# Performance work log

Hardware: AMD Instinct MI355X
Metric: run time of the kernel (lower is better)

The kernel has to match this reference:

```python
import jax, jax.numpy as jnp
import numpy as np

N_INIT = jnp.array([17.047, 14.099, 3.625], dtype=jnp.float32)
CA_INIT = jnp.array([16.967, 12.784, 4.338], dtype=jnp.float32)
C_INIT = jnp.array([15.685, 12.755, 5.133], dtype=jnp.float32)


def _unit(x):
    return x / (jnp.linalg.norm(x, axis=-1, keepdims=True) + 1e-8)


def _place_dihedral(a, b, c, bond_angle, bond_length, torsion):
    # a,b,c: [B,3]; bond_angle/bond_length/torsion: [B]
    ab = b - a
    bc = _unit(c - b)
    cr = jnp.cross(ab, bc)
    crn = jnp.linalg.norm(cr, axis=-1, keepdims=True)
    n_main = _unit(cr)
    # collinear fallback (per-element; almost never triggers for real angles)
    perp = jnp.zeros_like(bc).at[..., 0].set(1.0)
    ct = jnp.cross(bc, perp)
    ctn = jnp.linalg.norm(ct, axis=-1, keepdims=True)
    perp2 = jnp.where(ctn < 1e-6, jnp.zeros_like(bc).at[..., 1].set(1.0), perp)
    n_fb = _unit(jnp.cross(bc, perp2))
    n = jnp.where(crn < 1e-6, n_fb, n_main)
    nbc = jnp.cross(n, bc)
    m = jnp.stack([bc, nbc, n], axis=-1)  # [B,3,3]
    d_local = jnp.stack([
        -bond_length * jnp.cos(bond_angle),
        bond_length * jnp.cos(torsion) * jnp.sin(bond_angle),
        bond_length * jnp.sin(torsion) * jnp.sin(bond_angle),
    ], axis=-1)  # [B,3]
    d = jnp.einsum('bij,bj->bi', m, d_local)
    return d + c


def _nerf_build(phi, psi, omega, bond_lengths, bond_angles):
    B, L = phi.shape
    init = jnp.broadcast_to(jnp.stack([N_INIT, CA_INIT, C_INIT]), (B, 3, 3))
    # per-step params, leading axis = residue index i in [0, L-2]
    xs = (
        psi[:, :L - 1].T,                 # psi_i
        omega[:, :L - 1].T,               # omega_i
        phi[:, 1:].T,                     # phi_{i+1}
        bond_lengths[:, :L - 1, 2].T,     # C-N length
        bond_lengths[:, :L - 1, 0].T,     # N-CA length
        bond_lengths[:, :L - 1, 1].T,     # CA-C length
        bond_angles[:, :L - 1, 1].T,      # CA-C-N angle
        bond_angles[:, :L - 1, 2].T,      # C-N-CA angle
        bond_angles[:, :L - 1, 0].T,      # N-CA-C angle
    )

    def step(prev, x):
        psi_i, omega_i, phi_i, len_cn, len_nca, len_cac, ang_cacn, ang_cnca, ang_ncac = x
        a, b, c = prev[:, 0], prev[:, 1], prev[:, 2]
        n = _place_dihedral(a, b, c, ang_cacn, len_cn, psi_i)
        ca = _place_dihedral(b, c, n, ang_cnca, len_nca, omega_i)
        cc = _place_dihedral(c, n, ca, ang_ncac, len_cac, phi_i)
        new = jnp.stack([n, ca, cc], axis=1)  # [B,3,3]
        return new, new

    _, outs = jax.lax.scan(step, init, xs)  # [L-1,B,3,3]
    rest = outs.transpose(1, 0, 2, 3).reshape(B, 3 * (L - 1), 3)
    return jnp.concatenate([init, rest], axis=1)  # [B, 3L, 3]


def setup_inputs() -> dict:
    key = jax.random.key(0)
    k0, k1, k2, k3, k4 = jax.random.split(key, 5)
    B, L = 4096, 512
    phi = jax.random.normal(k0, (B, L), dtype=jnp.float32)
    psi = jax.random.normal(k1, (B, L), dtype=jnp.float32)
    omega = jax.random.normal(k2, (B, L), dtype=jnp.float32)
    # realistic positive bond lengths (~1.0-1.5 A) and bond angles (~1.5-2.3 rad)
    bond_lengths = 1.0 + 0.5 * jax.random.uniform(k3, (B, L, 3), dtype=jnp.float32)
    bond_angles = 1.5 + 0.8 * jax.random.uniform(k4, (B, L, 3), dtype=jnp.float32)
    return {"phi": phi, "psi": psi, "omega": omega,
            "bond_lengths": bond_lengths, "bond_angles": bond_angles}


def reference(phi, psi, omega, bond_lengths, bond_angles):
    return _nerf_build(phi, psi, omega, bond_lengths, bond_angles)
```

## Files before the change

kernel.cpp:

```cpp
#include <hip/hip_runtime.h>
#include <math.h>


struct Xform { float r[9]; float t[3]; };

__device__ __forceinline__ void xf_identity(Xform& A) {
  A.r[0]=1.f; A.r[1]=0.f; A.r[2]=0.f;
  A.r[3]=0.f; A.r[4]=1.f; A.r[5]=0.f;
  A.r[6]=0.f; A.r[7]=0.f; A.r[8]=1.f;
  A.t[0]=0.f; A.t[1]=0.f; A.t[2]=0.f;
}

__device__ __forceinline__ Xform xf_compose(const Xform& A, const Xform& B) {
  Xform C;
#pragma unroll
  for (int i = 0; i < 3; ++i) {
    float a0 = A.r[3*i+0], a1 = A.r[3*i+1], a2 = A.r[3*i+2];
    C.r[3*i+0] = a0*B.r[0] + a1*B.r[3] + a2*B.r[6];
    C.r[3*i+1] = a0*B.r[1] + a1*B.r[4] + a2*B.r[7];
    C.r[3*i+2] = a0*B.r[2] + a1*B.r[5] + a2*B.r[8];
    C.t[i]     = a0*B.t[0] + a1*B.t[1] + a2*B.t[2] + A.t[i];
  }
  return C;
}

__device__ __forceinline__ Xform xf_delta(float theta, float len, float tau) {
  float st, ct, sx, cx;
  __sincosf(theta, &st, &ct);
  __sincosf(tau, &sx, &cx);
  float ux = -ct, uy = cx*st, uz = sx*st;
  Xform D;
  D.r[0] = ux;     D.r[1] = -st;    D.r[2] = 0.f;
  D.r[3] = uy;     D.r[4] = -ct*cx; D.r[5] = -sx;
  D.r[6] = uz;     D.r[7] = -ct*sx; D.r[8] = cx;
  D.t[0] = len*ux; D.t[1] = len*uy; D.t[2] = len*uz;
  return D;
}

__device__ __forceinline__ void xf_store(float* p, const Xform& A) {
#pragma unroll
  for (int i = 0; i < 9; ++i) p[i] = A.r[i];
#pragma unroll
  for (int i = 0; i < 3; ++i) p[9+i] = A.t[i];
}
__device__ __forceinline__ void xf_load(const float* p, Xform& A) {
#pragma unroll
  for (int i = 0; i < 9; ++i) A.r[i] = p[i];
#pragma unroll
  for (int i = 0; i < 3; ++i) A.t[i] = p[9+i];
}

#define LCH 512
#define NRES 511
#define SCAN_STRIDE 13

static __device__ const float c_init[9] = {
  17.047f, 14.099f, 3.625f,
  16.967f, 12.784f, 4.338f,
  15.685f, 12.755f, 5.133f };

__global__ __launch_bounds__(256) void nerf_scan_kernel(
    const float* __restrict__ g_phi, const float* __restrict__ g_psi,
    const float* __restrict__ g_omg, const float* __restrict__ g_bl,
    const float* __restrict__ g_ba, float* __restrict__ g_out)
{
  __shared__ float s_psi[NRES];
  __shared__ float s_omg[NRES];
  __shared__ float s_phi[NRES];
  __shared__ float s_bl[3*NRES];
  __shared__ float s_ba[3*NRES];
  __shared__ float s_scan[256*SCAN_STRIDE];

  const int b = blockIdx.x;
  const int t = threadIdx.x;

  const float* phir = g_phi + (size_t)b*LCH;
  const float* psir = g_psi + (size_t)b*LCH;
  const float* omgr = g_omg + (size_t)b*LCH;
  const float* blr  = g_bl  + (size_t)b*LCH*3;
  const float* bar  = g_ba  + (size_t)b*LCH*3;

  for (int i = t; i < NRES; i += 256) {
    s_psi[i] = psir[i];
    s_omg[i] = omgr[i];
    s_phi[i] = phir[i+1];
  }
  for (int i = t; i < 3*NRES; i += 256) {
    s_bl[i] = blr[i];
    s_ba[i] = bar[i];
  }
  __syncthreads();

  Xform P; xf_identity(P);
#pragma unroll
  for (int e = 0; e < 2; ++e) {
    int j = 2*t + e;
    if (j < NRES) {
      P = xf_compose(P, xf_delta(s_ba[3*j+1], s_bl[3*j+2], s_psi[j]));
      P = xf_compose(P, xf_delta(s_ba[3*j+2], s_bl[3*j+0], s_omg[j]));
      P = xf_compose(P, xf_delta(s_ba[3*j+0], s_bl[3*j+1], s_phi[j]));
    }
  }
  xf_store(&s_scan[t*SCAN_STRIDE], P);
  __syncthreads();

  for (int d = 1; d < 256; d <<= 1) {
    Xform left;
    bool act = (t >= d);
    if (act) xf_load(&s_scan[(t-d)*SCAN_STRIDE], left);
    __syncthreads();
    if (act) {
      P = xf_compose(left, P);
      xf_store(&s_scan[t*SCAN_STRIDE], P);
    }
    __syncthreads();
  }

  Xform A;
  {
    const float ax=17.047f, ay=14.099f, az=3.625f;
    const float bx_=16.967f, by_=12.784f, bz_=4.338f;
    const float cx_=15.685f, cy_=12.755f, cz_=5.133f;
    float abx=bx_-ax, aby=by_-ay, abz=bz_-az;
    float vx=cx_-bx_, vy=cy_-by_, vz=cz_-bz_;
    float vn = sqrtf(vx*vx+vy*vy+vz*vz) + 1e-8f;
    vx/=vn; vy/=vn; vz/=vn;
    float crx = aby*vz - abz*vy;
    float cry = abz*vx - abx*vz;
    float crz = abx*vy - aby*vx;
    float cn = sqrtf(crx*crx+cry*cry+crz*crz) + 1e-8f;
    float nx=crx/cn, ny=cry/cn, nz=crz/cn;
    float mx = ny*vz - nz*vy;
    float my = nz*vx - nx*vz;
    float mz = nx*vy - ny*vx;
    Xform I0;
    I0.r[0]=vx; I0.r[1]=mx; I0.r[2]=nx;
    I0.r[3]=vy; I0.r[4]=my; I0.r[5]=ny;
    I0.r[6]=vz; I0.r[7]=mz; I0.r[8]=nz;
    I0.t[0]=cx_; I0.t[1]=cy_; I0.t[2]=cz_;
    if (t == 0) {
      A = I0;
    } else {
      Xform E; xf_load(&s_scan[(t-1)*SCAN_STRIDE], E);
      A = xf_compose(I0, E);
    }
  }

  float* orow = g_out + (size_t)b * (3*LCH) * 3;
  if (t < 9) orow[t] = c_init[t];

#pragma unroll
  for (int e = 0; e < 2; ++e) {
    int j = 2*t + e;
    if (j < NRES) {
      float* o = orow + (size_t)(3 + 3*j) * 3;
      A = xf_compose(A, xf_delta(s_ba[3*j+1], s_bl[3*j+2], s_psi[j]));
      o[0]=A.t[0]; o[1]=A.t[1]; o[2]=A.t[2];
      A = xf_compose(A, xf_delta(s_ba[3*j+2], s_bl[3*j+0], s_omg[j]));
      o[3]=A.t[0]; o[4]=A.t[1]; o[5]=A.t[2];
      A = xf_compose(A, xf_delta(s_ba[3*j+0], s_bl[3*j+1], s_phi[j]));
      o[6]=A.t[0]; o[7]=A.t[1]; o[8]=A.t[2];
    }
  }
}

extern "C" void kernel_launch(void* const* d_in, const int* in_sizes, int n_in,
                              void* d_out, int out_size, void* d_ws, size_t ws_size,
                              hipStream_t stream) {
  const float* phi = (const float*)d_in[0];
  const float* psi = (const float*)d_in[1];
  const float* omg = (const float*)d_in[2];
  const float* bl  = (const float*)d_in[3];
  const float* ba  = (const float*)d_in[4];
  float* out = (float*)d_out;
  const int B = in_sizes[0] / LCH;
  hipLaunchKernelGGL(nerf_scan_kernel, dim3(B), dim3(256), 0, stream,
                     phi, psi, omg, bl, ba, out);
}
```

Baseline: 168.6 us.

## Map one chain per wavefront with register-resident inputs and shuffle-based scan

Each 64-lane wavefront now handles a whole chain, with 8 residues per lane, instead of one 256-thread block per chain. Inputs are loaded with float4 into registers, and the block-level LDS scan with barriers is replaced by a wave-level scan using __shfl_up. Composing with each elementary transform is specialised into an in-place step that exploits the known zero entry. Each lane now does a serial chain of 24 steps twice, which raises register pressure and serial latency. Output stores per lane are strided rather than coalesced.

```diff
diff --git a/kernel.cpp b/kernel.cpp
--- a/kernel.cpp
+++ b/kernel.cpp
@@ -2,17 +2,14 @@
 #include <math.h>
 
 
-struct Xform { float r[9]; float t[3]; };
+#define LCH 512
+#define NRES 511
+#define RPL 8
 
-__device__ __forceinline__ void xf_identity(Xform& A) {
-  A.r[0]=1.f; A.r[1]=0.f; A.r[2]=0.f;
-  A.r[3]=0.f; A.r[4]=1.f; A.r[5]=0.f;
-  A.r[6]=0.f; A.r[7]=0.f; A.r[8]=1.f;
-  A.t[0]=0.f; A.t[1]=0.f; A.t[2]=0.f;
-}
+struct Xf { float r[9]; float t[3]; };
 
-__device__ __forceinline__ Xform xf_compose(const Xform& A, const Xform& B) {
-  Xform C;
+__device__ __forceinline__ Xf xf_compose(const Xf& A, const Xf& B) {
+  Xf C;
 #pragma unroll
   for (int i = 0; i < 3; ++i) {
     float a0 = A.r[3*i+0], a1 = A.r[3*i+1], a2 = A.r[3*i+2];
@@ -24,99 +21,121 @@
   return C;
 }
 
-__device__ __forceinline__ Xform xf_delta(float theta, float len, float tau) {
+__device__ __forceinline__ void xf_step(Xf& P, float theta, float len, float tau) {
   float st, ct, sx, cx;
   __sincosf(theta, &st, &ct);
   __sincosf(tau, &sx, &cx);
   float ux = -ct, uy = cx*st, uz = sx*st;
-  Xform D;
-  D.r[0] = ux;     D.r[1] = -st;    D.r[2] = 0.f;
-  D.r[3] = uy;     D.r[4] = -ct*cx; D.r[5] = -sx;
-  D.r[6] = uz;     D.r[7] = -ct*sx; D.r[8] = cx;
-  D.t[0] = len*ux; D.t[1] = len*uy; D.t[2] = len*uz;
-  return D;
+  float v0 = -st, v1 = -ct*cx, v2 = -ct*sx;
+  float c00 = P.r[0]*ux + P.r[1]*uy + P.r[2]*uz;
+  float c10 = P.r[3]*ux + P.r[4]*uy + P.r[5]*uz;
+  float c20 = P.r[6]*ux + P.r[7]*uy + P.r[8]*uz;
+  float c01 = P.r[0]*v0 + P.r[1]*v1 + P.r[2]*v2;
+  float c11 = P.r[3]*v0 + P.r[4]*v1 + P.r[5]*v2;
+  float c21 = P.r[6]*v0 + P.r[7]*v1 + P.r[8]*v2;
+  float c02 = P.r[2]*cx - P.r[1]*sx;
+  float c12 = P.r[5]*cx - P.r[4]*sx;
+  float c22 = P.r[8]*cx - P.r[7]*sx;
+  P.t[0] += len*c00; P.t[1] += len*c10; P.t[2] += len*c20;
+  P.r[0]=c00; P.r[1]=c01; P.r[2]=c02;
+  P.r[3]=c10; P.r[4]=c11; P.r[5]=c12;
+  P.r[6]=c20; P.r[7]=c21; P.r[8]=c22;
 }
 
-__device__ __forceinline__ void xf_store(float* p, const Xform& A) {
-#pragma unroll
-  for (int i = 0; i < 9; ++i) p[i] = A.r[i];
-#pragma unroll
-  for (int i = 0; i < 3; ++i) p[9+i] = A.t[i];
-}
-__device__ __forceinline__ void xf_load(const float* p, Xform& A) {
-#pragma unroll
-  for (int i = 0; i < 9; ++i) A.r[i] = p[i];
-#pragma unroll
-  for (int i = 0; i < 3; ++i) A.t[i] = p[9+i];
+__device__ __forceinline__ void xf_set_delta(Xf& P, float theta, float len, float tau) {
+  float st, ct, sx, cx;
+  __sincosf(theta, &st, &ct);
+  __sincosf(tau, &sx, &cx);
+  float ux = -ct, uy = cx*st, uz = sx*st;
+  P.r[0]=ux; P.r[1]=-st;    P.r[2]=0.f;
+  P.r[3]=uy; P.r[4]=-ct*cx; P.r[5]=-sx;
+  P.r[6]=uz; P.r[7]=-ct*sx; P.r[8]=cx;
+  P.t[0]=len*ux; P.t[1]=len*uy; P.t[2]=len*uz;
 }
 
-#define LCH 512
-#define NRES 511
-#define SCAN_STRIDE 13
+__device__ __forceinline__ Xf xf_shfl_up(const Xf& P, int d) {
+  Xf O;
+#pragma unroll
+  for (int i = 0; i < 9; ++i) O.r[i] = __shfl_up(P.r[i], d, 64);
+#pragma unroll
+  for (int i = 0; i < 3; ++i) O.t[i] = __shfl_up(P.t[i], d, 64);
+  return O;
+}
 
 static __device__ const float c_init[9] = {
   17.047f, 14.099f, 3.625f,
   16.967f, 12.784f, 4.338f,
   15.685f, 12.755f, 5.133f };
 
-__global__ __launch_bounds__(256) void nerf_scan_kernel(
+__global__ __launch_bounds__(256) void nerf_wavescan_kernel(
     const float* __restrict__ g_phi, const float* __restrict__ g_psi,
     const float* __restrict__ g_omg, const float* __restrict__ g_bl,
     const float* __restrict__ g_ba, float* __restrict__ g_out)
 {
-  __shared__ float s_psi[NRES];
-  __shared__ float s_omg[NRES];
-  __shared__ float s_phi[NRES];
-  __shared__ float s_bl[3*NRES];
-  __shared__ float s_ba[3*NRES];
-  __shared__ float s_scan[256*SCAN_STRIDE];
+  const int lane  = threadIdx.x & 63;
+  const int wave  = threadIdx.x >> 6;
+  const int chain = blockIdx.x * 4 + wave;
 
-  const int b = blockIdx.x;
-  const int t = threadIdx.x;
+  const float* phir = g_phi + (size_t)chain * LCH;
+  const float* psir = g_psi + (size_t)chain * LCH;
+  const float* omgr = g_omg + (size_t)chain * LCH;
+  const float* blr  = g_bl  + (size_t)chain * LCH * 3;
+  const float* bar  = g_ba  + (size_t)chain * LCH * 3;
 
-  const float* phir = g_phi + (size_t)b*LCH;
-  const float* psir = g_psi + (size_t)b*LCH;
-  const float* omgr = g_omg + (size_t)b*LCH;
-  const float* blr  = g_bl  + (size_t)b*LCH*3;
-  const float* bar  = g_ba  + (size_t)b*LCH*3;
+  const int j0 = lane * RPL;
 
-  for (int i = t; i < NRES; i += 256) {
-    s_psi[i] = psir[i];
-    s_omg[i] = omgr[i];
-    s_phi[i] = phir[i+1];
+  float psi_[RPL], omg_[RPL], phl_[RPL];
+  float bl_[3*RPL], ba_[3*RPL];
+  {
+    const float4* p;
+    p = (const float4*)(psir + j0);
+#pragma unroll
+    for (int q = 0; q < RPL/4; ++q) { float4 v = p[q];
+      psi_[4*q]=v.x; psi_[4*q+1]=v.y; psi_[4*q+2]=v.z; psi_[4*q+3]=v.w; }
+    p = (const float4*)(omgr + j0);
+#pragma unroll
+    for (int q = 0; q < RPL/4; ++q) { float4 v = p[q];
+      omg_[4*q]=v.x; omg_[4*q+1]=v.y; omg_[4*q+2]=v.z; omg_[4*q+3]=v.w; }
+    p = (const float4*)(phir + j0);
+#pragma unroll
+    for (int q = 0; q < RPL/4; ++q) { float4 v = p[q];
+      phl_[4*q]=v.x; phl_[4*q+1]=v.y; phl_[4*q+2]=v.z; phl_[4*q+3]=v.w; }
+    p = (const float4*)(blr + (size_t)j0*3);
+#pragma unroll
+    for (int q = 0; q < (3*RPL)/4; ++q) { float4 v = p[q];
+      bl_[4*q]=v.x; bl_[4*q+1]=v.y; bl_[4*q+2]=v.z; bl_[4*q+3]=v.w; }
+    p = (const float4*)(bar + (size_t)j0*3);
+#pragma unroll
+    for (int q = 0; q < (3*RPL)/4; ++q) { float4 v = p[q];
+      ba_[4*q]=v.x; ba_[4*q+1]=v.y; ba_[4*q+2]=v.z; ba_[4*q+3]=v.w; }
   }
-  for (int i = t; i < 3*NRES; i += 256) {
-    s_bl[i] = blr[i];
-    s_ba[i] = bar[i];
-  }
-  __syncthreads();
+  float phi_next = __shfl_down(phl_[0], 1, 64);
+  float phiN[RPL];
+#pragma unroll
+  for (int e = 0; e < RPL-1; ++e) phiN[e] = phl_[e+1];
+  phiN[RPL-1] = phi_next;
 
-  Xform P; xf_identity(P);
+  Xf P;
+  xf_set_delta(P, ba_[1], bl_[2], psi_[0]);
+  xf_step(P, ba_[2], bl_[0], omg_[0]);
+  xf_step(P, ba_[0], bl_[1], phiN[0]);
 #pragma unroll
-  for (int e = 0; e < 2; ++e) {
-    int j = 2*t + e;
-    if (j < NRES) {
-      P = xf_compose(P, xf_delta(s_ba[3*j+1], s_bl[3*j+2], s_psi[j]));
-      P = xf_compose(P, xf_delta(s_ba[3*j+2], s_bl[3*j+0], s_omg[j]));
-      P = xf_compose(P, xf_delta(s_ba[3*j+0], s_bl[3*j+1], s_phi[j]));
+  for (int e = 1; e < RPL; ++e) {
+    if (j0 + e < NRES) {
+      xf_step(P, ba_[3*e+1], bl_[3*e+2], psi_[e]);
+      xf_step(P, ba_[3*e+2], bl_[3*e+0], omg_[e]);
+      xf_step(P, ba_[3*e+0], bl_[3*e+1], phiN[e]);
     }
   }
-  xf_store(&s_scan[t*SCAN_STRIDE], P);
-  __syncthreads();
 
-  for (int d = 1; d < 256; d <<= 1) {
-    Xform left;
-    bool act = (t >= d);
-    if (act) xf_load(&s_scan[(t-d)*SCAN_STRIDE], left);
-    __syncthreads();
-    if (act) {
-      P = xf_compose(left, P);
-      xf_store(&s_scan[t*SCAN_STRIDE], P);
-    }
-    __syncthreads();
+#pragma unroll
+  for (int d = 1; d < 64; d <<= 1) {
+    Xf O = xf_shfl_up(P, d);
+    if (lane >= d) P = xf_compose(O, P);
   }
 
-  Xform A;
+  Xf E = xf_shfl_up(P, 1);
+  Xf A;
   {
     const float ax=17.047f, ay=14.099f, az=3.625f;
     const float bx_=16.967f, by_=12.784f, bz_=4.338f;
@@ -133,32 +152,27 @@
     float mx = ny*vz - nz*vy;
     float my = nz*vx - nx*vz;
     float mz = nx*vy - ny*vx;
-    Xform I0;
+    Xf I0;
     I0.r[0]=vx; I0.r[1]=mx; I0.r[2]=nx;
     I0.r[3]=vy; I0.r[4]=my; I0.r[5]=ny;
     I0.r[6]=vz; I0.r[7]=mz; I0.r[8]=nz;
     I0.t[0]=cx_; I0.t[1]=cy_; I0.t[2]=cz_;
-    if (t == 0) {
-      A = I0;
-    } else {
-      Xform E; xf_load(&s_scan[(t-1)*SCAN_STRIDE], E);
-      A = xf_compose(I0, E);
-    }
+    A = (lane == 0) ? I0 : xf_compose(I0, E);
   }
 
-  float* orow = g_out + (size_t)b * (3*LCH) * 3;
-  if (t < 9) orow[t] = c_init[t];
+  float* orow = g_out + (size_t)chain * (3*LCH) * 3;
+  if (lane < 9) orow[lane] = c_init[lane];
 
 #pragma unroll
-  for (int e = 0; e < 2; ++e) {
-    int j = 2*t + e;
+  for (int e = 0; e < RPL; ++e) {
+    int j = j0 + e;
     if (j < NRES) {
       float* o = orow + (size_t)(3 + 3*j) * 3;
-      A = xf_compose(A, xf_delta(s_ba[3*j+1], s_bl[3*j+2], s_psi[j]));
+      xf_step(A, ba_[3*e+1], bl_[3*e+2], psi_[e]);
       o[0]=A.t[0]; o[1]=A.t[1]; o[2]=A.t[2];
-      A = xf_compose(A, xf_delta(s_ba[3*j+2], s_bl[3*j+0], s_omg[j]));
+      xf_step(A, ba_[3*e+2], bl_[3*e+0], omg_[e]);
       o[3]=A.t[0]; o[4]=A.t[1]; o[5]=A.t[2];
-      A = xf_compose(A, xf_delta(s_ba[3*j+0], s_bl[3*j+1], s_phi[j]));
+      xf_step(A, ba_[3*e+0], bl_[3*e+1], phiN[e]);
       o[6]=A.t[0]; o[7]=A.t[1]; o[8]=A.t[2];
     }
   }
@@ -174,6 +188,6 @@
   const float* ba  = (const float*)d_in[4];
   float* out = (float*)d_out;
   const int B = in_sizes[0] / LCH;
-  hipLaunchKernelGGL(nerf_scan_kernel, dim3(B), dim3(256), 0, stream,
+  hipLaunchKernelGGL(nerf_wavescan_kernel, dim3(B / 4), dim3(256), 0, stream,
                      phi, psi, omg, bl, ba, out);
 }
```

New measurement: 171.5 us. No clear change (+1.7%).
